# Performance work log

Measured on AMD Instinct MI355X. Metric: run time of the kernel, lower is better.

The kernel has to match this reference:

```python
import jax, jax.numpy as jnp
import numpy as np

LK = 8  # db4 has 8 taps
LEVEL = 5
# pywt.Wavelet('db4').filter_bank[0] == dec_lo
DB4_LO = np.array([-0.010597401784997278, 0.032883011666982945, 0.030841381835986965,
                   -0.18703481171888114, -0.02798376941698385, 0.6308807679295904,
                   0.7148465705525415, 0.23037781330885523], dtype=np.float32)
DN = ('NCH', 'OIH', 'NCH')


def _wpt_kernels(level):
    # Filter_Free WPT: distinct kernel per child node; parent j even -> (lp, hp), odd -> (hp, lp)
    cmf = (-1.0) ** np.arange(LK)
    k_lp = DB4_LO
    k_hp = (DB4_LO[::-1] * cmf).astype(np.float32)
    ks = []
    for i in range(level):
        rows = []
        for j in range(2 ** i):
            rows += [k_lp, k_hp] if j % 2 == 0 else [k_hp, k_lp]
        ks.append(jnp.asarray(np.stack(rows)))  # [2^(i+1), LK]
    return ks


def setup_inputs() -> dict:
    key = jax.random.key(0)
    kx, kb = jax.random.split(key)
    B, N = 128, 32768
    inp = {'x': jax.random.normal(kx, (B, 1, N), dtype=jnp.float32)}
    for i, K in enumerate(_wpt_kernels(LEVEL)):
        inp[f'k{i + 1}'] = K
    for i in range(LEVEL):
        kb, sub = jax.random.split(kb)
        # small positive thresholds (Act_Init=0 would make the threshold an exact identity)
        inp[f'b{i + 1}'] = 0.1 * jax.random.uniform(sub, (2 ** (i + 1),), dtype=jnp.float32)
    return inp


def _analysis(c, K, b):
    # c: [B, G, M] parents -> [B, 2G, M//2] children; one grouped 8-tap conv for the whole level
    G = c.shape[1]
    cp = jnp.pad(c, ((0, 0), (0, 0), (LK // 2 - 1, LK // 2)))
    y = jax.lax.conv_general_dilated(cp, K[:, None, :], (2,), 'VALID',
                                     feature_group_count=G, dimension_numbers=DN)
    bb = b[None, :, None]
    # symmetric sigmoid soft-threshold (Thresh_SigSym), fused elementwise
    return y * (jax.nn.sigmoid(10.0 * (y - bb)) + jax.nn.sigmoid(-10.0 * (y + bb)))


def _synthesis(y, K):
    # adjoint of the strided analysis conv (conv_transpose): [B, 2G, M] -> [B, G, 2M]
    G = y.shape[1] // 2
    M = y.shape[2]
    W = jnp.flip(K, -1).reshape(G, 2, LK)  # sum the two children of each parent
    out = jax.lax.conv_general_dilated(y, W, (1,), [(LK - 1, LK - 1)], lhs_dilation=(2,),
                                       feature_group_count=G, dimension_numbers=DN)
    pl = LK // 2 - 1  # undo analysis left pad
    return out[:, :, pl:pl + 2 * M]


def reference(x, k1, k2, k3, k4, k5, b1, b2, b3, b4, b5):
    Ks = [k1, k2, k3, k4, k5]
    bs = [b1, b2, b3, b4, b5]
    c = x  # [B, 1, N]
    for K, b in zip(Ks, bs):
        c = _analysis(c, K, b)
    for K in Ks[::-1]:
        c = _synthesis(c, K)
    return c  # [B, 1, N] reconstruction
```

## Files before the change

### kernel.cpp

```cpp
#include <hip/hip_runtime.h>

#define TPB 512

constexpr int NSEQ = 32768;
constexpr int C0   = 4096;
constexpr int COLW = 576;
constexpr float SCG = 14.4269504089f;


typedef float f2 __attribute__((ext_vector_type(2)));

__device__ __forceinline__ f2 sp(float x) { return (f2){x, x}; }
__device__ __forceinline__ f2 fma2(f2 a, f2 b, f2 c) { return __builtin_elementwise_fma(a, b, c); }

__device__ __forceinline__ float4 ldf4(const float* p) { return *reinterpret_cast<const float4*>(p); }
__device__ __forceinline__ void   stf4(float* p, const float4 v) { *reinterpret_cast<float4*>(p) = v; }

__device__ __forceinline__ float rfl(float x) {
    return __builtin_bit_cast(float, __builtin_amdgcn_readfirstlane(__builtin_bit_cast(int, x)));
}

__device__ __forceinline__ f2 gated2(f2 y, f2 tb) {
    f2 t1 = fma2(y, sp(-SCG), tb);
    f2 t2 = fma2(y, sp( SCG), tb);
    f2 s;
    s[0] = __builtin_amdgcn_rcpf(1.f + __builtin_amdgcn_exp2f(t1[0]))
         + __builtin_amdgcn_rcpf(1.f + __builtin_amdgcn_exp2f(t2[0]));
    s[1] = __builtin_amdgcn_rcpf(1.f + __builtin_amdgcn_exp2f(t1[1]))
         + __builtin_amdgcn_rcpf(1.f + __builtin_amdgcn_exp2f(t2[1]));
    return y * s;
}

template<int LEin, int P, int PAIRS, int Nlev, bool EDGE, int OUTSTRIDE, int EOOFF>
__device__ __forceinline__ void analysis8(
    const float* __restrict__ in, float* __restrict__ out,
    const f2* __restrict__ klh, const float* __restrict__ bias, int outBase)
{
    constexpr int TPC = P / 8;
    constexpr int TOT = PAIRS * TPC;
    static_assert(TOT <= TPB, "analysis phase must be single-generation");
    const int task = threadIdx.x;
    if (task < TOT) {
        const int c  = task / TPC;
        const int i0 = (task - c * TPC) * 8;

        const float* pe = in + c * (2 * LEin) + i0;
        const float* po = pe + LEin;
        float a[12], b[12];
        reinterpret_cast<float4*>(a)[0] = ldf4(pe);
        reinterpret_cast<float4*>(a)[1] = ldf4(pe + 4);
        reinterpret_cast<float4*>(a)[2] = ldf4(pe + 8);
        reinterpret_cast<float4*>(b)[0] = ldf4(po);
        reinterpret_cast<float4*>(b)[1] = ldf4(po + 4);
        reinterpret_cast<float4*>(b)[2] = ldf4(po + 8);

        const int sw    = c & 1;
        const int ch_lp = 2 * c + sw;
        const int ch_hp = 2 * c + 1 - sw;
        const f2  tb    = (f2){bias[ch_lp], bias[ch_hp]};

        const int j0 = i0 >> 1;
        float* ol = out + ch_lp * OUTSTRIDE;
        float* oh = out + ch_hp * OUTSTRIDE;

#pragma unroll
        for (int par = 0; par < 2; ++par) {
            f2 w[4];
#pragma unroll
            for (int k = 0; k < 4; ++k) {
                const int r = 2 * k + par;
                f2 y = (f2){0.f, 0.f};
#pragma unroll
                for (int u = 0; u < 4; ++u) {
                    y = fma2(sp(a[r + u]), klh[2 * u], y);
                    y = fma2(sp(b[r + u]), klh[2 * u + 1], y);
                }
                y = gated2(y, tb);
                if (EDGE) {
                    const bool ok = ((unsigned)(outBase + i0 + r) < (unsigned)Nlev);
                    y[0] = ok ? y[0] : 0.f;
                    y[1] = ok ? y[1] : 0.f;
                }
                w[k] = y;
            }
            stf4(ol + par * EOOFF + j0, make_float4(w[0][0], w[1][0], w[2][0], w[3][0]));
            stf4(oh + par * EOOFF + j0, make_float4(w[0][1], w[1][1], w[2][1], w[3][1]));
        }
    }
}

template<int JROFF, bool EDGE>
__device__ __forceinline__ void synth_core(
    const float* __restrict__ ya, const float* __restrict__ yb,
    const f2* __restrict__ lrev, const f2* __restrict__ hrev,
    int gpos, int Nlev, float* __restrict__ o)
{
    f2 p1 = (f2){0.f, 0.f}, p2 = (f2){0.f, 0.f}, p3 = (f2){0.f, 0.f};
    float o0 = 0.f, o7 = 0.f;
#pragma unroll
    for (int q = 0; q < 4; ++q) {
        const f2 cl = lrev[q], ch = hrev[q];
        o0 = fmaf(ya[JROFF + q],     cl[1], o0);
        o0 = fmaf(yb[JROFF + q],     ch[1], o0);
        o7 = fmaf(ya[JROFF + 4 + q], cl[0], o7);
        o7 = fmaf(yb[JROFF + 4 + q], ch[0], o7);
        p1 = fma2(sp(ya[JROFF + 1 + q]), cl, p1);
        p1 = fma2(sp(yb[JROFF + 1 + q]), ch, p1);
        p2 = fma2(sp(ya[JROFF + 2 + q]), cl, p2);
        p2 = fma2(sp(yb[JROFF + 2 + q]), ch, p2);
        p3 = fma2(sp(ya[JROFF + 3 + q]), cl, p3);
        p3 = fma2(sp(yb[JROFF + 3 + q]), ch, p3);
    }
    o[0] = o0;    o[1] = p1[0]; o[2] = p1[1]; o[3] = p2[0];
    o[4] = p2[1]; o[5] = p3[0]; o[6] = p3[1]; o[7] = o7;
    if (EDGE) {
#pragma unroll
        for (int r = 0; r < 8; ++r) {
            const bool ok = ((unsigned)(gpos + r) < (unsigned)Nlev);
            o[r] = ok ? o[r] : 0.f;
        }
    }
}

template<int INSTRIDE, int Sout, int G, int Nlev, bool EDGE>
__device__ __forceinline__ void synthN(
    const float* __restrict__ in, float* __restrict__ out,
    const f2* __restrict__ lrev, const f2* __restrict__ hrev, int outBase)
{
    constexpr int TPG = Sout / 8;
    constexpr int TOT = G * TPG;
    static_assert(TOT <= 2 * TPB, "synth phase must fit in two generations");
#pragma unroll
    for (int t = threadIdx.x; t < TOT; t += TPB) {
        const int g   = t / TPG;
        const int nl0 = (t - g * TPG) * 8;
        const int sw  = g & 1;

        float ya[8], yb[8];
        {
            const float* p0 = in + (2 * g + sw)     * INSTRIDE + nl0 / 2;
            const float* p1 = in + (2 * g + 1 - sw) * INSTRIDE + nl0 / 2;
            reinterpret_cast<float4*>(ya)[0] = ldf4(p0);
            reinterpret_cast<float4*>(ya)[1] = ldf4(p0 + 4);
            reinterpret_cast<float4*>(yb)[0] = ldf4(p1);
            reinterpret_cast<float4*>(yb)[1] = ldf4(p1 + 4);
        }
        float o[8];
        synth_core<0, EDGE>(ya, yb, lrev, hrev, outBase + nl0, Nlev, o);
        float* op = out + g * Sout + nl0;
        stf4(op,     make_float4(o[0], o[1], o[2], o[3]));
        stf4(op + 4, make_float4(o[4], o[5], o[6], o[7]));
    }
}

template<bool EDGE>
__device__ __forceinline__ void stretch_wave(
    float* __restrict__ bufA, float* __restrict__ bufB,
    const f2* __restrict__ klh, const f2* __restrict__ lrev, const f2* __restrict__ hrev,
    const float* __restrict__ bss, int s)
{
    const int w    = threadIdx.x >> 6;
    const int lane = threadIdx.x & 63;
    float* colA = bufA + w * COLW;
    float* colB = bufB + w * COLW;
    const int sww = w & 1;

    if (lane < 35) {
        const int i0 = lane * 8;
        const float* pe = colB + i0;
        const float* po = pe + 284;
        float a[12], b[12];
        reinterpret_cast<float4*>(a)[0] = ldf4(pe);
        reinterpret_cast<float4*>(a)[1] = ldf4(pe + 4);
        reinterpret_cast<float4*>(a)[2] = ldf4(pe + 8);
        reinterpret_cast<float4*>(b)[0] = ldf4(po);
        reinterpret_cast<float4*>(b)[1] = ldf4(po + 4);
        reinterpret_cast<float4*>(b)[2] = ldf4(po + 8);
        const f2 tb = (f2){bss[14 + 2 * w + sww], bss[14 + 2 * w + 1 - sww]};
        const int j0 = i0 >> 1;
        float* ol = colA + sww * 280;
        float* oh = colA + (1 - sww) * 280;
#pragma unroll
        for (int par = 0; par < 2; ++par) {
            f2 v[4];
#pragma unroll
            for (int k = 0; k < 4; ++k) {
                const int r = 2 * k + par;
                f2 y = (f2){0.f, 0.f};
#pragma unroll
                for (int u = 0; u < 4; ++u) {
                    y = fma2(sp(a[r + u]), klh[2 * u], y);
                    y = fma2(sp(b[r + u]), klh[2 * u + 1], y);
                }
                y = gated2(y, tb);
                if (EDGE) {
                    const bool ok = ((unsigned)(((s >> 4) - 11) + i0 + r) < 2048u);
                    y[0] = ok ? y[0] : 0.f;
                    y[1] = ok ? y[1] : 0.f;
                }
                v[k] = y;
            }
            stf4(ol + par * 140 + j0, make_float4(v[0][0], v[1][0], v[2][0], v[3][0]));
            stf4(oh + par * 140 + j0, make_float4(v[0][1], v[1][1], v[2][1], v[3][1]));
        }
    }

    if (lane < 34) {
        const int l  = (lane >= 17) ? 1 : 0;
        const int i0 = (lane - 17 * l) * 8;
        const float* pe = colA + l * 280 + i0;
        const float* po = pe + 140;
        float a[12], b[12];
        reinterpret_cast<float4*>(a)[0] = ldf4(pe);
        reinterpret_cast<float4*>(a)[1] = ldf4(pe + 4);
        reinterpret_cast<float4*>(a)[2] = ldf4(pe + 8);
        reinterpret_cast<float4*>(b)[0] = ldf4(po);
        reinterpret_cast<float4*>(b)[1] = ldf4(po + 4);
        reinterpret_cast<float4*>(b)[2] = ldf4(po + 8);
        const int cg = 2 * w + l;
        const f2 tb = (f2){bss[30 + 2 * cg + l], bss[30 + 2 * cg + 1 - l]};
        f2 v[8];
#pragma unroll
        for (int r = 0; r < 8; ++r) {
            f2 y = (f2){0.f, 0.f};
#pragma unroll
            for (int u = 0; u < 4; ++u) {
                y = fma2(sp(a[r + u]), klh[2 * u], y);
                y = fma2(sp(b[r + u]), klh[2 * u + 1], y);
            }
            y = gated2(y, tb);
            if (EDGE) {
                const bool ok = ((unsigned)(((s >> 5) - 4) + i0 + r) < 1024u);
                y[0] = ok ? y[0] : 0.f;
                y[1] = ok ? y[1] : 0.f;
            }
            v[r] = y;
        }
        float* plo = colB + (3 * l) * 136 + i0;
        float* phi = colB + (l + 1) * 136 + i0;
        stf4(plo,     make_float4(v[0][0], v[1][0], v[2][0], v[3][0]));
        stf4(plo + 4, make_float4(v[4][0], v[5][0], v[6][0], v[7][0]));
        stf4(phi,     make_float4(v[0][1], v[1][1], v[2][1], v[3][1]));
        stf4(phi + 4, make_float4(v[4][1], v[5][1], v[6][1], v[7][1]));
    }

#pragma unroll
    for (int t = lane; t < 66; t += 64) {
        const int gl  = (t >= 33) ? 1 : 0;
        const int nl0 = (t - 33 * gl) * 8;
        const float* p0 = colB + (3 * gl) * 136 + nl0 / 2;
        const float* p1 = colB + (gl + 1) * 136 + nl0 / 2;
        float ya[8], yb[8];
        reinterpret_cast<float4*>(ya)[0] = ldf4(p0);
        reinterpret_cast<float4*>(ya)[1] = ldf4(p0 + 4);
        reinterpret_cast<float4*>(yb)[0] = ldf4(p1);
        reinterpret_cast<float4*>(yb)[1] = ldf4(p1 + 4);
        float o[8];
        synth_core<0, EDGE>(ya, yb, lrev, hrev, ((s >> 4) - 4) + nl0, 2048, o);
        float* op = colA + gl * 264 + nl0;
        stf4(op,     make_float4(o[0], o[1], o[2], o[3]));
        stf4(op + 4, make_float4(o[4], o[5], o[6], o[7]));
    }

#pragma unroll
    for (int t = lane; t < 65; t += 64) {
        const int nl0 = t * 8;
        const float* p0 = colA + sww * 264 + nl0 / 2;
        const float* p1 = colA + (1 - sww) * 264 + nl0 / 2;
        float ya[8], yb[8];
        reinterpret_cast<float4*>(ya)[0] = ldf4(p0);
        reinterpret_cast<float4*>(ya)[1] = ldf4(p0 + 4);
        reinterpret_cast<float4*>(yb)[0] = ldf4(p1);
        reinterpret_cast<float4*>(yb)[1] = ldf4(p1 + 4);
        float o[8];
        synth_core<0, EDGE>(ya, yb, lrev, hrev, ((s >> 3) - 4) + nl0, 4096, o);
        stf4(colB + nl0,     make_float4(o[0], o[1], o[2], o[3]));
        stf4(colB + nl0 + 4, make_float4(o[4], o[5], o[6], o[7]));
    }
}

template<bool EDGE>
__device__ __forceinline__ void run_chunk(
    const float* __restrict__ xb, float* __restrict__ ob, int s,
    float* __restrict__ bufA, float* __restrict__ bufB,
    const f2* __restrict__ klh, const f2* __restrict__ lrev, const f2* __restrict__ hrev,
    const float* __restrict__ bss)
{
    const int tid = threadIdx.x;

    {
        const int base = s - 221;
#pragma unroll
        for (int k = 0; k < 5; ++k) {
            const int j = tid + TPB * k;
            if (j < 2300) {
                const int g0 = base + 2 * j;
                if (EDGE) {
                    bufA[j]        = ((unsigned)g0       < (unsigned)NSEQ) ? xb[g0]     : 0.f;
                    bufA[2300 + j] = ((unsigned)(g0 + 1) < (unsigned)NSEQ) ? xb[g0 + 1] : 0.f;
                } else {
                    bufA[j]        = xb[g0];
                    bufA[2300 + j] = xb[g0 + 1];
                }
            }
        }
    }
    __syncthreads();

    analysis8<2300, 2296, 1, 16384, EDGE, 2296, 1148>(bufA, bufB, klh, bss + 0, (s >> 1) - 109);
    __syncthreads();
    analysis8<1148, 1144, 2,  8192, EDGE, 1144,  572>(bufB, bufA, klh, bss + 2, (s >> 2) - 53);
    __syncthreads();
    analysis8< 572,  568, 4,  4096, EDGE, COLW,  284>(bufA, bufB, klh, bss + 6, (s >> 3) - 25);
    __syncthreads();

    stretch_wave<EDGE>(bufA, bufB, klh, lrev, hrev, bss, s);
    __syncthreads();

    synthN<COLW, 1032, 4,  8192, EDGE>(bufB, bufA, lrev, hrev, (s >> 2) - 4);
    __syncthreads();
    synthN<1032, 2056, 2, 16384, EDGE>(bufA, bufB, lrev, hrev, (s >> 1) - 4);
    __syncthreads();

    {
        const int i0 = tid * 8;
        float ya[12], yb[12];
        {
            const float* p0 = bufB + i0 / 2;
            const float* p1 = p0 + 2056;
            reinterpret_cast<float4*>(ya)[0] = ldf4(p0);
            reinterpret_cast<float4*>(ya)[1] = ldf4(p0 + 4);
            reinterpret_cast<float4*>(ya)[2] = ldf4(p0 + 8);
            reinterpret_cast<float4*>(yb)[0] = ldf4(p1);
            reinterpret_cast<float4*>(yb)[1] = ldf4(p1 + 4);
            reinterpret_cast<float4*>(yb)[2] = ldf4(p1 + 8);
        }
        float o[8];
        synth_core<2, false>(ya, yb, lrev, hrev, 0, 1 << 30, o);
        stf4(ob + i0,     make_float4(o[0], o[1], o[2], o[3]));
        stf4(ob + i0 + 4, make_float4(o[4], o[5], o[6], o[7]));
    }
}

__global__ __launch_bounds__(TPB, 8) void wpt_fused(
    const float* __restrict__ x,
    const float* __restrict__ K1, const float* __restrict__ K2,
    const float* __restrict__ K3, const float* __restrict__ K4,
    const float* __restrict__ K5,
    const float* __restrict__ B1, const float* __restrict__ B2,
    const float* __restrict__ B3, const float* __restrict__ B4,
    const float* __restrict__ B5,
    float* __restrict__ out)
{
    __shared__ __align__(16) float bufA[4608];
    __shared__ __align__(16) float bufB[4608];
    __shared__ float bss[62];

    const int tid   = threadIdx.x;
    const int batch = blockIdx.x >> 3;
    const int cid   = blockIdx.x & 7;
    const int s     = cid * C0;

    float lp[8], hp[8];
#pragma unroll
    for (int t = 0; t < 8; ++t) {
        lp[t] = rfl(K1[t]);
        hp[t] = rfl(K1[8 + t]);
    }
    f2 klh[8], lrev[4], hrev[4];
#pragma unroll
    for (int t = 0; t < 8; ++t) klh[t] = (f2){lp[t], hp[t]};
#pragma unroll
    for (int q = 0; q < 4; ++q) {
        lrev[q] = (f2){lp[6 - 2 * q], lp[7 - 2 * q]};
        hrev[q] = (f2){hp[6 - 2 * q], hp[7 - 2 * q]};
    }

    {
        const float* bin[5] = {B1, B2, B3, B4, B5};
        const int boff[5] = {0, 2, 6, 14, 30};
#pragma unroll
        for (int l = 0; l < 5; ++l)
            for (int i = tid; i < (2 << l); i += TPB) bss[boff[l] + i] = SCG * bin[l][i];
    }

    const float* xb = x + batch * NSEQ;
    float* ob = out + batch * NSEQ + s;

    if (cid == 0 || cid == 7)
        run_chunk<true >(xb, ob, s, bufA, bufB, klh, lrev, hrev, bss);
    else
        run_chunk<false>(xb, ob, s, bufA, bufB, klh, lrev, hrev, bss);
}

extern "C" void kernel_launch(void* const* d_in, const int* in_sizes, int n_in,
                              void* d_out, int out_size, void* d_ws, size_t ws_size,
                              hipStream_t stream) {
    const int nbatch = in_sizes[0] / NSEQ;
    wpt_fused<<<dim3(nbatch * (NSEQ / C0)), dim3(TPB), 0, stream>>>(
        (const float*)d_in[0],
        (const float*)d_in[1], (const float*)d_in[2],
        (const float*)d_in[3], (const float*)d_in[4],
        (const float*)d_in[5],
        (const float*)d_in[6], (const float*)d_in[7],
        (const float*)d_in[8], (const float*)d_in[9],
        (const float*)d_in[10],
        (float*)d_out);
}
```

Measured before the change: 113.1 us.

## Replace per-wave stretch phase with block-wide levels and vectorize input load

Removes the wave-private stretch_wave routine that handled analysis levels 4-5 and synthesis levels 5-4 without block barriers. Those levels now run as ordinary block-wide analysis8/synthN phases separated by __syncthreads, with a LAST variant for the deepest analysis level. The input load now reads float4 from global memory and de-interleaves even/odd samples into LDS instead of doing scalar strided loads. This trades the barrier-free per-wave work for four extra block barriers and the under-occupancy of small phases, while cutting the number of global load instructions.

```diff
diff --git a/kernel.cpp b/kernel.cpp
--- a/kernel.cpp
+++ b/kernel.cpp
@@ -4,7 +4,6 @@
 
 constexpr int NSEQ = 32768;
 constexpr int C0   = 4096;
-constexpr int COLW = 576;
 constexpr float SCG = 14.4269504089f;
 
 
@@ -31,7 +30,7 @@
     return y * s;
 }
 
-template<int LEin, int P, int PAIRS, int Nlev, bool EDGE, int OUTSTRIDE, int EOOFF>
+template<int LEin, int P, int PAIRS, int Nlev, bool EDGE, int OUTSTRIDE, int EOOFF, bool LAST = false>
 __device__ __forceinline__ void analysis8(
     const float* __restrict__ in, float* __restrict__ out,
     const f2* __restrict__ klh, const float* __restrict__ bias, int outBase)
@@ -59,16 +58,10 @@
         const int ch_hp = 2 * c + 1 - sw;
         const f2  tb    = (f2){bias[ch_lp], bias[ch_hp]};
 
-        const int j0 = i0 >> 1;
-        float* ol = out + ch_lp * OUTSTRIDE;
-        float* oh = out + ch_hp * OUTSTRIDE;
-
-#pragma unroll
-        for (int par = 0; par < 2; ++par) {
-            f2 w[4];
-#pragma unroll
-            for (int k = 0; k < 4; ++k) {
-                const int r = 2 * k + par;
+        if (LAST) {
+            f2 v[8];
+#pragma unroll
+            for (int r = 0; r < 8; ++r) {
                 f2 y = (f2){0.f, 0.f};
 #pragma unroll
                 for (int u = 0; u < 4; ++u) {
@@ -81,10 +74,41 @@
                     y[0] = ok ? y[0] : 0.f;
                     y[1] = ok ? y[1] : 0.f;
                 }
-                w[k] = y;
+                v[r] = y;
             }
-            stf4(ol + par * EOOFF + j0, make_float4(w[0][0], w[1][0], w[2][0], w[3][0]));
-            stf4(oh + par * EOOFF + j0, make_float4(w[0][1], w[1][1], w[2][1], w[3][1]));
+            float* ol = out + ch_lp * OUTSTRIDE + i0;
+            float* oh = out + ch_hp * OUTSTRIDE + i0;
+            stf4(ol,     make_float4(v[0][0], v[1][0], v[2][0], v[3][0]));
+            stf4(ol + 4, make_float4(v[4][0], v[5][0], v[6][0], v[7][0]));
+            stf4(oh,     make_float4(v[0][1], v[1][1], v[2][1], v[3][1]));
+            stf4(oh + 4, make_float4(v[4][1], v[5][1], v[6][1], v[7][1]));
+        } else {
+            const int j0 = i0 >> 1;
+            float* ol = out + ch_lp * OUTSTRIDE + j0;
+            float* oh = out + ch_hp * OUTSTRIDE + j0;
+#pragma unroll
+            for (int par = 0; par < 2; ++par) {
+                f2 w[4];
+#pragma unroll
+                for (int k = 0; k < 4; ++k) {
+                    const int r = 2 * k + par;
+                    f2 y = (f2){0.f, 0.f};
+#pragma unroll
+                    for (int u = 0; u < 4; ++u) {
+                        y = fma2(sp(a[r + u]), klh[2 * u], y);
+                        y = fma2(sp(b[r + u]), klh[2 * u + 1], y);
+                    }
+                    y = gated2(y, tb);
+                    if (EDGE) {
+                        const bool ok = ((unsigned)(outBase + i0 + 2 * k + par) < (unsigned)Nlev);
+                        y[0] = ok ? y[0] : 0.f;
+                        y[1] = ok ? y[1] : 0.f;
+                    }
+                    w[k] = y;
+                }
+                stf4(ol + par * EOOFF, make_float4(w[0][0], w[1][0], w[2][0], w[3][0]));
+                stf4(oh + par * EOOFF, make_float4(w[0][1], w[1][1], w[2][1], w[3][1]));
+            }
         }
     }
 }
@@ -136,146 +160,19 @@
         const int nl0 = (t - g * TPG) * 8;
         const int sw  = g & 1;
 
+        const float* p0 = in + (2 * g + sw)     * INSTRIDE + nl0 / 2;
+        const float* p1 = in + (2 * g + 1 - sw) * INSTRIDE + nl0 / 2;
         float ya[8], yb[8];
-        {
-            const float* p0 = in + (2 * g + sw)     * INSTRIDE + nl0 / 2;
-            const float* p1 = in + (2 * g + 1 - sw) * INSTRIDE + nl0 / 2;
-            reinterpret_cast<float4*>(ya)[0] = ldf4(p0);
-            reinterpret_cast<float4*>(ya)[1] = ldf4(p0 + 4);
-            reinterpret_cast<float4*>(yb)[0] = ldf4(p1);
-            reinterpret_cast<float4*>(yb)[1] = ldf4(p1 + 4);
-        }
+        reinterpret_cast<float4*>(ya)[0] = ldf4(p0);
+        reinterpret_cast<float4*>(ya)[1] = ldf4(p0 + 4);
+        reinterpret_cast<float4*>(yb)[0] = ldf4(p1);
+        reinterpret_cast<float4*>(yb)[1] = ldf4(p1 + 4);
+
         float o[8];
         synth_core<0, EDGE>(ya, yb, lrev, hrev, outBase + nl0, Nlev, o);
         float* op = out + g * Sout + nl0;
         stf4(op,     make_float4(o[0], o[1], o[2], o[3]));
         stf4(op + 4, make_float4(o[4], o[5], o[6], o[7]));
-    }
-}
-
-template<bool EDGE>
-__device__ __forceinline__ void stretch_wave(
-    float* __restrict__ bufA, float* __restrict__ bufB,
-    const f2* __restrict__ klh, const f2* __restrict__ lrev, const f2* __restrict__ hrev,
-    const float* __restrict__ bss, int s)
-{
-    const int w    = threadIdx.x >> 6;
-    const int lane = threadIdx.x & 63;
-    float* colA = bufA + w * COLW;
-    float* colB = bufB + w * COLW;
-    const int sww = w & 1;
-
-    if (lane < 35) {
-        const int i0 = lane * 8;
-        const float* pe = colB + i0;
-        const float* po = pe + 284;
-        float a[12], b[12];
-        reinterpret_cast<float4*>(a)[0] = ldf4(pe);
-        reinterpret_cast<float4*>(a)[1] = ldf4(pe + 4);
-        reinterpret_cast<float4*>(a)[2] = ldf4(pe + 8);
-        reinterpret_cast<float4*>(b)[0] = ldf4(po);
-        reinterpret_cast<float4*>(b)[1] = ldf4(po + 4);
-        reinterpret_cast<float4*>(b)[2] = ldf4(po + 8);
-        const f2 tb = (f2){bss[14 + 2 * w + sww], bss[14 + 2 * w + 1 - sww]};
-        const int j0 = i0 >> 1;
-        float* ol = colA + sww * 280;
-        float* oh = colA + (1 - sww) * 280;
-#pragma unroll
-        for (int par = 0; par < 2; ++par) {
-            f2 v[4];
-#pragma unroll
-            for (int k = 0; k < 4; ++k) {
-                const int r = 2 * k + par;
-                f2 y = (f2){0.f, 0.f};
-#pragma unroll
-                for (int u = 0; u < 4; ++u) {
-                    y = fma2(sp(a[r + u]), klh[2 * u], y);
-                    y = fma2(sp(b[r + u]), klh[2 * u + 1], y);
-                }
-                y = gated2(y, tb);
-                if (EDGE) {
-                    const bool ok = ((unsigned)(((s >> 4) - 11) + i0 + r) < 2048u);
-                    y[0] = ok ? y[0] : 0.f;
-                    y[1] = ok ? y[1] : 0.f;
-                }
-                v[k] = y;
-            }
-            stf4(ol + par * 140 + j0, make_float4(v[0][0], v[1][0], v[2][0], v[3][0]));
-            stf4(oh + par * 140 + j0, make_float4(v[0][1], v[1][1], v[2][1], v[3][1]));
-        }
-    }
-
-    if (lane < 34) {
-        const int l  = (lane >= 17) ? 1 : 0;
-        const int i0 = (lane - 17 * l) * 8;
-        const float* pe = colA + l * 280 + i0;
-        const float* po = pe + 140;
-        float a[12], b[12];
-        reinterpret_cast<float4*>(a)[0] = ldf4(pe);
-        reinterpret_cast<float4*>(a)[1] = ldf4(pe + 4);
-        reinterpret_cast<float4*>(a)[2] = ldf4(pe + 8);
-        reinterpret_cast<float4*>(b)[0] = ldf4(po);
-        reinterpret_cast<float4*>(b)[1] = ldf4(po + 4);
-        reinterpret_cast<float4*>(b)[2] = ldf4(po + 8);
-        const int cg = 2 * w + l;
-        const f2 tb = (f2){bss[30 + 2 * cg + l], bss[30 + 2 * cg + 1 - l]};
-        f2 v[8];
-#pragma unroll
-        for (int r = 0; r < 8; ++r) {
-            f2 y = (f2){0.f, 0.f};
-#pragma unroll
-            for (int u = 0; u < 4; ++u) {
-                y = fma2(sp(a[r + u]), klh[2 * u], y);
-                y = fma2(sp(b[r + u]), klh[2 * u + 1], y);
-            }
-            y = gated2(y, tb);
-            if (EDGE) {
-                const bool ok = ((unsigned)(((s >> 5) - 4) + i0 + r) < 1024u);
-                y[0] = ok ? y[0] : 0.f;
-                y[1] = ok ? y[1] : 0.f;
-            }
-            v[r] = y;
-        }
-        float* plo = colB + (3 * l) * 136 + i0;
-        float* phi = colB + (l + 1) * 136 + i0;
-        stf4(plo,     make_float4(v[0][0], v[1][0], v[2][0], v[3][0]));
-        stf4(plo + 4, make_float4(v[4][0], v[5][0], v[6][0], v[7][0]));
-        stf4(phi,     make_float4(v[0][1], v[1][1], v[2][1], v[3][1]));
-        stf4(phi + 4, make_float4(v[4][1], v[5][1], v[6][1], v[7][1]));
-    }
-
-#pragma unroll
-    for (int t = lane; t < 66; t += 64) {
-        const int gl  = (t >= 33) ? 1 : 0;
-        const int nl0 = (t - 33 * gl) * 8;
-        const float* p0 = colB + (3 * gl) * 136 + nl0 / 2;
-        const float* p1 = colB + (gl + 1) * 136 + nl0 / 2;
-        float ya[8], yb[8];
-        reinterpret_cast<float4*>(ya)[0] = ldf4(p0);
-        reinterpret_cast<float4*>(ya)[1] = ldf4(p0 + 4);
-        reinterpret_cast<float4*>(yb)[0] = ldf4(p1);
-        reinterpret_cast<float4*>(yb)[1] = ldf4(p1 + 4);
-        float o[8];
-        synth_core<0, EDGE>(ya, yb, lrev, hrev, ((s >> 4) - 4) + nl0, 2048, o);
-        float* op = colA + gl * 264 + nl0;
-        stf4(op,     make_float4(o[0], o[1], o[2], o[3]));
-        stf4(op + 4, make_float4(o[4], o[5], o[6], o[7]));
-    }
-
-#pragma unroll
-    for (int t = lane; t < 65; t += 64) {
-        const int nl0 = t * 8;
-        const float* p0 = colA + sww * 264 + nl0 / 2;
-        const float* p1 = colA + (1 - sww) * 264 + nl0 / 2;
-        float ya[8], yb[8];
-        reinterpret_cast<float4*>(ya)[0] = ldf4(p0);
-        reinterpret_cast<float4*>(ya)[1] = ldf4(p0 + 4);
-        reinterpret_cast<float4*>(yb)[0] = ldf4(p1);
-        reinterpret_cast<float4*>(yb)[1] = ldf4(p1 + 4);
-        float o[8];
-        synth_core<0, EDGE>(ya, yb, lrev, hrev, ((s >> 3) - 4) + nl0, 4096, o);
-        stf4(colB + nl0,     make_float4(o[0], o[1], o[2], o[3]));
-        stf4(colB + nl0 + 4, make_float4(o[4], o[5], o[6], o[7]));
     }
 }
 
@@ -290,36 +187,50 @@
 
     {
         const int base = s - 221;
-#pragma unroll
-        for (int k = 0; k < 5; ++k) {
-            const int j = tid + TPB * k;
-            if (j < 2300) {
-                const int g0 = base + 2 * j;
-                if (EDGE) {
-                    bufA[j]        = ((unsigned)g0       < (unsigned)NSEQ) ? xb[g0]     : 0.f;
-                    bufA[2300 + j] = ((unsigned)(g0 + 1) < (unsigned)NSEQ) ? xb[g0 + 1] : 0.f;
+        const int a0   = base - 3;
+#pragma unroll
+        for (int k = 0; k < 3; ++k) {
+            const int q = tid + TPB * k;
+            if (q < 1151) {
+                const int a = a0 + 4 * q;
+                float4 v;
+                if (!EDGE || (a >= 0 && a + 3 < NSEQ)) {
+                    v = ldf4(xb + a);
                 } else {
-                    bufA[j]        = xb[g0];
-                    bufA[2300 + j] = xb[g0 + 1];
+                    v.x = ((unsigned)(a)     < (unsigned)NSEQ) ? xb[a]     : 0.f;
+                    v.y = ((unsigned)(a + 1) < (unsigned)NSEQ) ? xb[a + 1] : 0.f;
+                    v.z = ((unsigned)(a + 2) < (unsigned)NSEQ) ? xb[a + 2] : 0.f;
+                    v.w = ((unsigned)(a + 3) < (unsigned)NSEQ) ? xb[a + 3] : 0.f;
                 }
+                const int jo = 2 * q - 2;
+                const int je = 2 * q - 1;
+                if ((unsigned)jo       < 2300u) bufA[2304 + jo]     = v.x;
+                if ((unsigned)je       < 2300u) bufA[je]            = v.y;
+                if ((unsigned)(jo + 1) < 2300u) bufA[2304 + jo + 1] = v.z;
+                if ((unsigned)(je + 1) < 2300u) bufA[je + 1]        = v.w;
             }
         }
     }
     __syncthreads();
 
-    analysis8<2300, 2296, 1, 16384, EDGE, 2296, 1148>(bufA, bufB, klh, bss + 0, (s >> 1) - 109);
-    __syncthreads();
-    analysis8<1148, 1144, 2,  8192, EDGE, 1144,  572>(bufB, bufA, klh, bss + 2, (s >> 2) - 53);
-    __syncthreads();
-    analysis8< 572,  568, 4,  4096, EDGE, COLW,  284>(bufA, bufB, klh, bss + 6, (s >> 3) - 25);
-    __syncthreads();
-
-    stretch_wave<EDGE>(bufA, bufB, klh, lrev, hrev, bss, s);
-    __syncthreads();
-
-    synthN<COLW, 1032, 4,  8192, EDGE>(bufB, bufA, lrev, hrev, (s >> 2) - 4);
-    __syncthreads();
-    synthN<1032, 2056, 2, 16384, EDGE>(bufA, bufB, lrev, hrev, (s >> 1) - 4);
+    analysis8<2304, 2296,  1, 16384, EDGE, 2296, 1148>(bufA, bufB, klh, bss + 0,  (s >> 1) - 109);
+    __syncthreads();
+    analysis8<1148, 1144,  2,  8192, EDGE, 1144,  572>(bufB, bufA, klh, bss + 2,  (s >> 2) - 53);
+    __syncthreads();
+    analysis8< 572,  568,  4,  4096, EDGE,  568,  284>(bufA, bufB, klh, bss + 6,  (s >> 3) - 25);
+    __syncthreads();
+    analysis8< 284,  280,  8,  2048, EDGE,  280,  140>(bufB, bufA, klh, bss + 14, (s >> 4) - 11);
+    __syncthreads();
+    analysis8< 140,  136, 16,  1024, EDGE,  136,    0, true>(bufA, bufB, klh, bss + 30, (s >> 5) - 4);
+    __syncthreads();
+
+    synthN< 136,  264, 16,  2048, EDGE>(bufB, bufA, lrev, hrev, (s >> 4) - 4);
+    __syncthreads();
+    synthN< 264,  520,  8,  4096, EDGE>(bufA, bufB, lrev, hrev, (s >> 3) - 4);
+    __syncthreads();
+    synthN< 520, 1032,  4,  8192, EDGE>(bufB, bufA, lrev, hrev, (s >> 2) - 4);
+    __syncthreads();
+    synthN<1032, 2056,  2, 16384, EDGE>(bufA, bufB, lrev, hrev, (s >> 1) - 4);
     __syncthreads();
 
     {
```

New measurement: 111.9 us. Within noise of the previous version (-1.0%).
